# Kernel tuning notes

Hardware: AMD Instinct MI355X
Metric: run time of the kernel (lower is better)

The kernel has to match this reference:

```python
import jax, jax.numpy as jnp
import numpy as np

EPS = 1e-8  # torch F.cosine_similarity clamps each norm to eps

def setup_inputs() -> dict:
    key = jax.random.key(0)
    frames, height, width, hidden = 64, 23, 24, 1152
    total = frames * height * width  # 35328 image tokens
    hidden_states = jax.random.normal(key, (total, hidden), dtype=jnp.float32)
    return {
        "hidden_states": hidden_states,
        "frames": frames,
        "height": height,
        "width": width,
        "interval": 1,
    }

def _cos(a, b):
    dot = jnp.sum(a * b, axis=-1)
    na = jnp.maximum(jnp.linalg.norm(a, axis=-1), EPS)
    nb = jnp.maximum(jnp.linalg.norm(b, axis=-1), EPS)
    return dot / (na * nb)

def reference(hidden_states, frames, height, width, interval):
    # Faithful vectorized form of compute_token_similarities_vectorized:
    # for each frame f < frames-interval,
    #   right[f, i] = cos(x[f, i], x[f+interval, i+1])     for i in [0, tpf-2]
    #   down [f, i] = cos(x[f, i], x[f+interval, i+width]) for i in [0, tpf-width-1]
    # all other positions stay -1.
    tpf = height * width
    d = hidden_states.shape[-1]
    x = hidden_states.reshape(frames, tpf, d)
    valid = frames - interval

    right = _cos(x[:valid, : tpf - 1], x[interval:, 1:])            # [valid, tpf-1]
    down = _cos(x[:valid, : tpf - width], x[interval:, width:])      # [valid, tpf-width]

    right_full = jnp.full((frames, tpf), -1.0, dtype=hidden_states.dtype)
    right_full = right_full.at[:valid, : tpf - 1].set(right).reshape(-1)
    down_full = jnp.full((frames, tpf), -1.0, dtype=hidden_states.dtype)
    down_full = down_full.at[:valid, : tpf - width].set(down).reshape(-1)
    return right_full, down_full
```

## Files before the change

### kernel.cpp

```cpp
#include <hip/hip_runtime.h>
#include <math.h>

#define EPS 1e-8f

__global__ void __launch_bounds__(256) simdiff_kernel(
    const float* __restrict__ x,
    const int* __restrict__ p_frames,
    const int* __restrict__ p_width,
    const int* __restrict__ p_interval,
    float* __restrict__ out,
    int ntok, int hidden)
{
    const int frames   = *p_frames;
    const int width    = *p_width;
    const int interval = *p_interval;
    const int tpf      = ntok / frames;
    const int valid_f  = frames - interval;

    const int lane            = threadIdx.x & 63;
    const int wave_in_block   = threadIdx.x >> 6;
    const int waves_per_block = blockDim.x >> 6;
    const int stride          = gridDim.x * waves_per_block;
    const int nvec            = hidden >> 2;

    for (int task = blockIdx.x * waves_per_block + wave_in_block;
         task < ntok; task += stride) {
        const int f = task / tpf;
        const int i = task - f * tpf;

        const bool rv = (f < valid_f) && (i < tpf - 1);
        const bool dv = (f < valid_f) && (i < tpf - width);

        float out_r = -1.0f, out_d = -1.0f;

        if (rv || dv) {
            const float4* __restrict__ A =
                (const float4*)(x + (size_t)task * hidden);
            const float4* __restrict__ B1 = rv
                ? (const float4*)(x + (size_t)((f + interval) * tpf + i + 1) * hidden)
                : (const float4*)A;
            const float4* __restrict__ B2 = dv
                ? (const float4*)(x + (size_t)((f + interval) * tpf + i + width) * hidden)
                : (const float4*)A;

            float na2 = 0.f, nb1 = 0.f, nb2 = 0.f, d1 = 0.f, d2 = 0.f;

            for (int v = lane; v < nvec; v += 64) {
                const float4 a = A[v];
                na2 = fmaf(a.x, a.x, fmaf(a.y, a.y, fmaf(a.z, a.z, fmaf(a.w, a.w, na2))));
                if (rv) {
                    const float4 b = B1[v];
                    nb1 = fmaf(b.x, b.x, fmaf(b.y, b.y, fmaf(b.z, b.z, fmaf(b.w, b.w, nb1))));
                    d1  = fmaf(a.x, b.x, fmaf(a.y, b.y, fmaf(a.z, b.z, fmaf(a.w, b.w, d1))));
                }
                if (dv) {
                    const float4 c = B2[v];
                    nb2 = fmaf(c.x, c.x, fmaf(c.y, c.y, fmaf(c.z, c.z, fmaf(c.w, c.w, nb2))));
                    d2  = fmaf(a.x, c.x, fmaf(a.y, c.y, fmaf(a.z, c.z, fmaf(a.w, c.w, d2))));
                }
            }

            #pragma unroll
            for (int m = 1; m < 64; m <<= 1) {
                na2 += __shfl_xor(na2, m, 64);
                nb1 += __shfl_xor(nb1, m, 64);
                nb2 += __shfl_xor(nb2, m, 64);
                d1  += __shfl_xor(d1, m, 64);
                d2  += __shfl_xor(d2, m, 64);
            }

            const float na = fmaxf(sqrtf(na2), EPS);
            if (rv) out_r = d1 / (na * fmaxf(sqrtf(nb1), EPS));
            if (dv) out_d = d2 / (na * fmaxf(sqrtf(nb2), EPS));
        }

        if (lane == 0) {
            out[task]        = out_r;
            out[ntok + task] = out_d;
        }
    }
}

extern "C" void kernel_launch(void* const* d_in, const int* in_sizes, int n_in,
                              void* d_out, int out_size, void* d_ws, size_t ws_size,
                              hipStream_t stream) {
    const float* x        = (const float*)d_in[0];
    const int* p_frames   = (const int*)d_in[1];
    const int* p_width    = (const int*)d_in[3];
    const int* p_interval = (const int*)d_in[4];
    float* out            = (float*)d_out;

    const int ntok   = out_size / 2;
    const int hidden = in_sizes[0] / ntok;

    const int threads         = 256;
    const int waves_per_block = threads / 64;
    const int blocks          = (ntok + waves_per_block - 1) / waves_per_block;

    simdiff_kernel<<<blocks, threads, 0, stream>>>(
        x, p_frames, p_width, p_interval, out, ntok, hidden);
}
```

Baseline: 235.7 us.

## Add shape-specialized chain kernel reusing row loads and norms across tokens

Adds a kernel specialized for the 64x23x24x1152 shape. Each wave walks a diagonal chain of tokens, stepping by 23, so the B row used for the down neighbour becomes the next right neighbour and its norm is reused. Rows are loaded fully into registers with prefetch of the next rows. The aim is fewer redundant global loads and norm computations. In exchange it hardcodes dimensions with runtime fallbacks, and the generic kernel now loads B rows without the validity predicates.

```diff
diff --git a/kernel.cpp b/kernel.cpp
--- a/kernel.cpp
+++ b/kernel.cpp
@@ -3,7 +3,144 @@
 
 #define EPS 1e-8f
 
-__global__ void __launch_bounds__(256) simdiff_kernel(
+#define TPF   552
+#define HID   1152
+#define NTOK  35328
+#define WID   24
+#define NCHAINW 2898
+#define NBLK  726
+
+
+struct Row { float4 a, b, c, d; float2 e; };
+
+__device__ __forceinline__ Row load_row(const float* __restrict__ p, int lane) {
+    Row r;
+    const float4* p4 = (const float4*)p;
+    r.a = p4[lane];       r.b = p4[lane + 64];
+    r.c = p4[lane + 128]; r.d = p4[lane + 192];
+    r.e = ((const float2*)(p + 1024))[lane];
+    return r;
+}
+
+__device__ __forceinline__ float dotrr(const Row& x, const Row& y) {
+    float s = 0.f;
+    s = fmaf(x.a.x, y.a.x, s); s = fmaf(x.a.y, y.a.y, s);
+    s = fmaf(x.a.z, y.a.z, s); s = fmaf(x.a.w, y.a.w, s);
+    s = fmaf(x.b.x, y.b.x, s); s = fmaf(x.b.y, y.b.y, s);
+    s = fmaf(x.b.z, y.b.z, s); s = fmaf(x.b.w, y.b.w, s);
+    s = fmaf(x.c.x, y.c.x, s); s = fmaf(x.c.y, y.c.y, s);
+    s = fmaf(x.c.z, y.c.z, s); s = fmaf(x.c.w, y.c.w, s);
+    s = fmaf(x.d.x, y.d.x, s); s = fmaf(x.d.y, y.d.y, s);
+    s = fmaf(x.d.z, y.d.z, s); s = fmaf(x.d.w, y.d.w, s);
+    s = fmaf(x.e.x, y.e.x, s); s = fmaf(x.e.y, y.e.y, s);
+    return s;
+}
+
+__device__ __forceinline__ float reduce64(float v) {
+    #pragma unroll
+    for (int m = 1; m < 64; m <<= 1) v += __shfl_xor(v, m, 64);
+    return v;
+}
+
+__global__ void __launch_bounds__(256) simdiff_chain_kernel(
+    const float* __restrict__ x,
+    const int* __restrict__ p_frames,
+    const int* __restrict__ p_width,
+    const int* __restrict__ p_interval,
+    float* __restrict__ out)
+{
+    const int frames   = *p_frames;
+    const int width    = *p_width;
+    const int interval = *p_interval;
+    const int lane     = threadIdx.x & 63;
+    const int w        = blockIdx.x * (blockDim.x >> 6) + (threadIdx.x >> 6);
+
+    const bool spec = (frames == 64) && (width == WID) && (interval == 1);
+
+    if (spec) {
+        if (w >= NCHAINW) {
+            for (int i = (w - NCHAINW) * 64 + lane; i < 2 * TPF; i += 6 * 64) {
+                if (i < TPF) out[63 * TPF + i]          = -1.f;
+                else         out[NTOK + 63 * TPF + (i - TPF)] = -1.f;
+            }
+            return;
+        }
+        const int seg    = w & 1;
+        const int chain  = w >> 1;
+        const int f      = chain / 23;
+        const int c0     = chain - f * 23;
+        const int cstart = c0 + 276 * seg;
+
+        const float* xf  = x + (size_t)(f * TPF) * HID;
+        const float* xf1 = x + (size_t)((f + 1) * TPF) * HID;
+
+        Row bcur = load_row(xf1 + (size_t)(cstart + 1)  * HID, lane);
+        Row bnxt = load_row(xf1 + (size_t)(cstart + 24) * HID, lane);
+        Row acur = load_row(xf  + (size_t)cstart        * HID, lane);
+        float nbcur = reduce64(dotrr(bcur, bcur));
+
+        #pragma unroll
+        for (int j = 0; j < 12; ++j) {
+            const int c = cstart + 23 * j;
+
+            Row anxt = {}; Row bn2 = {};
+            if (j < 11) {
+                anxt = load_row(xf + (size_t)(c + 23) * HID, lane);
+                const int b2col = c + 47;
+                if (b2col < TPF)
+                    bn2 = load_row(xf1 + (size_t)b2col * HID, lane);
+            }
+
+            float na    = reduce64(dotrr(acur, acur));
+            float d1    = reduce64(dotrr(acur, bcur));
+            float d2    = reduce64(dotrr(acur, bnxt));
+            float nbnxt = reduce64(dotrr(bnxt, bnxt));
+
+            if (lane == 0) {
+                const int t  = f * TPF + c;
+                const float sa = fmaxf(sqrtf(na), EPS);
+                out[t]        = (c < TPF - 1)
+                    ? d1 / (sa * fmaxf(sqrtf(nbcur), EPS)) : -1.f;
+                out[NTOK + t] = (c < TPF - WID)
+                    ? d2 / (sa * fmaxf(sqrtf(nbnxt), EPS)) : -1.f;
+            }
+            nbcur = nbnxt; acur = anxt; bcur = bnxt; bnxt = bn2;
+        }
+        return;
+    }
+
+    const int ntok    = NTOK;
+    const int tpf     = ntok / frames;
+    const int valid_f = frames - interval;
+    const int stride  = gridDim.x * (blockDim.x >> 6);
+    for (int task = w; task < ntok; task += stride) {
+        const int f = task / tpf;
+        const int i = task - f * tpf;
+        const bool rv = (f < valid_f) && (i < tpf - 1);
+        const bool dv = (f < valid_f) && (i < tpf - width);
+        float out_r = -1.f, out_d = -1.f;
+        if (rv || dv) {
+            const float* A  = x + (size_t)task * HID;
+            const float* B1 = rv ? x + (size_t)((f + interval) * tpf + i + 1) * HID : A;
+            const float* B2 = dv ? x + (size_t)((f + interval) * tpf + i + width) * HID : A;
+            Row a = load_row(A, lane), b1 = load_row(B1, lane), b2 = load_row(B2, lane);
+            float na  = reduce64(dotrr(a, a));
+            float nb1 = reduce64(dotrr(b1, b1));
+            float nb2 = reduce64(dotrr(b2, b2));
+            float d1  = reduce64(dotrr(a, b1));
+            float d2  = reduce64(dotrr(a, b2));
+            const float sa = fmaxf(sqrtf(na), EPS);
+            if (rv) out_r = d1 / (sa * fmaxf(sqrtf(nb1), EPS));
+            if (dv) out_d = d2 / (sa * fmaxf(sqrtf(nb2), EPS));
+        }
+        if (lane == 0) {
+            out[task]        = out_r;
+            out[ntok + task] = out_d;
+        }
+    }
+}
+
+__global__ void __launch_bounds__(256) simdiff_generic_kernel(
     const float* __restrict__ x,
     const int* __restrict__ p_frames,
     const int* __restrict__ p_width,
@@ -16,50 +153,32 @@
     const int interval = *p_interval;
     const int tpf      = ntok / frames;
     const int valid_f  = frames - interval;
-
-    const int lane            = threadIdx.x & 63;
-    const int wave_in_block   = threadIdx.x >> 6;
-    const int waves_per_block = blockDim.x >> 6;
-    const int stride          = gridDim.x * waves_per_block;
-    const int nvec            = hidden >> 2;
-
-    for (int task = blockIdx.x * waves_per_block + wave_in_block;
+    const int lane     = threadIdx.x & 63;
+    const int stride   = gridDim.x * (blockDim.x >> 6);
+    const int nvec     = hidden >> 2;
+
+    for (int task = blockIdx.x * (blockDim.x >> 6) + (threadIdx.x >> 6);
          task < ntok; task += stride) {
         const int f = task / tpf;
         const int i = task - f * tpf;
-
         const bool rv = (f < valid_f) && (i < tpf - 1);
         const bool dv = (f < valid_f) && (i < tpf - width);
-
-        float out_r = -1.0f, out_d = -1.0f;
-
+        float out_r = -1.f, out_d = -1.f;
         if (rv || dv) {
-            const float4* __restrict__ A =
-                (const float4*)(x + (size_t)task * hidden);
-            const float4* __restrict__ B1 = rv
-                ? (const float4*)(x + (size_t)((f + interval) * tpf + i + 1) * hidden)
-                : (const float4*)A;
-            const float4* __restrict__ B2 = dv
-                ? (const float4*)(x + (size_t)((f + interval) * tpf + i + width) * hidden)
-                : (const float4*)A;
-
+            const float4* A  = (const float4*)(x + (size_t)task * hidden);
+            const float4* B1 = rv ? (const float4*)(x + (size_t)((f + interval) * tpf + i + 1) * hidden) : A;
+            const float4* B2 = dv ? (const float4*)(x + (size_t)((f + interval) * tpf + i + width) * hidden) : A;
             float na2 = 0.f, nb1 = 0.f, nb2 = 0.f, d1 = 0.f, d2 = 0.f;
-
             for (int v = lane; v < nvec; v += 64) {
                 const float4 a = A[v];
-                na2 = fmaf(a.x, a.x, fmaf(a.y, a.y, fmaf(a.z, a.z, fmaf(a.w, a.w, na2))));
-                if (rv) {
-                    const float4 b = B1[v];
-                    nb1 = fmaf(b.x, b.x, fmaf(b.y, b.y, fmaf(b.z, b.z, fmaf(b.w, b.w, nb1))));
-                    d1  = fmaf(a.x, b.x, fmaf(a.y, b.y, fmaf(a.z, b.z, fmaf(a.w, b.w, d1))));
-                }
-                if (dv) {
-                    const float4 c = B2[v];
-                    nb2 = fmaf(c.x, c.x, fmaf(c.y, c.y, fmaf(c.z, c.z, fmaf(c.w, c.w, nb2))));
-                    d2  = fmaf(a.x, c.x, fmaf(a.y, c.y, fmaf(a.z, c.z, fmaf(a.w, c.w, d2))));
-                }
-            }
-
+                na2 = fmaf(a.x,a.x, fmaf(a.y,a.y, fmaf(a.z,a.z, fmaf(a.w,a.w, na2))));
+                const float4 b = B1[v];
+                nb1 = fmaf(b.x,b.x, fmaf(b.y,b.y, fmaf(b.z,b.z, fmaf(b.w,b.w, nb1))));
+                d1  = fmaf(a.x,b.x, fmaf(a.y,b.y, fmaf(a.z,b.z, fmaf(a.w,b.w, d1))));
+                const float4 cc = B2[v];
+                nb2 = fmaf(cc.x,cc.x, fmaf(cc.y,cc.y, fmaf(cc.z,cc.z, fmaf(cc.w,cc.w, nb2))));
+                d2  = fmaf(a.x,cc.x, fmaf(a.y,cc.y, fmaf(a.z,cc.z, fmaf(a.w,cc.w, d2))));
+            }
             #pragma unroll
             for (int m = 1; m < 64; m <<= 1) {
                 na2 += __shfl_xor(na2, m, 64);
@@ -68,12 +187,10 @@
                 d1  += __shfl_xor(d1, m, 64);
                 d2  += __shfl_xor(d2, m, 64);
             }
-
-            const float na = fmaxf(sqrtf(na2), EPS);
-            if (rv) out_r = d1 / (na * fmaxf(sqrtf(nb1), EPS));
-            if (dv) out_d = d2 / (na * fmaxf(sqrtf(nb2), EPS));
-        }
-
+            const float sa = fmaxf(sqrtf(na2), EPS);
+            if (rv) out_r = d1 / (sa * fmaxf(sqrtf(nb1), EPS));
+            if (dv) out_d = d2 / (sa * fmaxf(sqrtf(nb2), EPS));
+        }
         if (lane == 0) {
             out[task]        = out_r;
             out[ntok + task] = out_d;
@@ -93,10 +210,12 @@
     const int ntok   = out_size / 2;
     const int hidden = in_sizes[0] / ntok;
 
-    const int threads         = 256;
-    const int waves_per_block = threads / 64;
-    const int blocks          = (ntok + waves_per_block - 1) / waves_per_block;
-
-    simdiff_kernel<<<blocks, threads, 0, stream>>>(
-        x, p_frames, p_width, p_interval, out, ntok, hidden);
-}
+    if (ntok == NTOK && hidden == HID) {
+        simdiff_chain_kernel<<<NBLK, 256, 0, stream>>>(
+            x, p_frames, p_width, p_interval, out);
+    } else {
+        const int blocks = (ntok + 3) / 4;
+        simdiff_generic_kernel<<<blocks, 256, 0, stream>>>(
+            x, p_frames, p_width, p_interval, out, ntok, hidden);
+    }
+}
```

Result: no change. 235.9 us (+0.1%).
